# Kernel optimization log

Measured on AMD Instinct MI355X. Metric: run time of the kernel, lower is better.

The kernel has to match this reference:

```python
import jax, jax.numpy as jnp
import numpy as np

N_NODES = 100000
N_EDGES = 1600000
D = 128

def setup_inputs() -> dict:
    key = jax.random.key(0)
    ks = jax.random.split(key, 8)
    s = 1.0 / np.sqrt(D)
    x = jax.random.normal(ks[0], (N_NODES, D), dtype=jnp.float32)
    edge_index = jax.random.randint(ks[1], (2, N_EDGES), 0, N_NODES, dtype=jnp.int64)
    Wl1 = jax.random.normal(ks[2], (D, D), dtype=jnp.float32) * s
    Wr1 = jax.random.normal(ks[3], (D, D), dtype=jnp.float32) * s
    b1 = jax.random.normal(ks[4], (D,), dtype=jnp.float32) * s
    Wl2 = jax.random.normal(ks[5], (D, D), dtype=jnp.float32) * s
    Wr2 = jax.random.normal(ks[6], (D, D), dtype=jnp.float32) * s
    b2 = jax.random.normal(ks[7], (D,), dtype=jnp.float32) * s
    return {"x": x, "edge_index": edge_index, "Wl1": Wl1, "Wr1": Wr1, "b1": b1,
            "Wl2": Wl2, "Wr2": Wr2, "b2": b2}

def _sage_mean(x, src, dst, n, Wl, Wr, b):
    # mean-aggregate neighbor features onto destination nodes
    msg = x[src]                                      # [E, D] gather
    agg = jax.ops.segment_sum(msg, dst, num_segments=n)  # [N, D] scatter-add
    deg = jax.ops.segment_sum(jnp.ones((src.shape[0],), x.dtype), dst, num_segments=n)
    mean = agg / jnp.maximum(deg, 1.0)[:, None]
    # SAGEConv: lin_l(aggregated) + lin_r(self), bias on lin_l
    return mean @ Wl.T + x @ Wr.T + b

def reference(x, edge_index, Wl1, Wr1, b1, Wl2, Wr2, b2):
    src, dst = edge_index[0], edge_index[1]
    n = x.shape[0]
    h = _sage_mean(x, src, dst, n, Wl1, Wr1, b1)
    h = jax.nn.relu(h)
    return _sage_mean(h, src, dst, n, Wl2, Wr2, b2)
```

## Files before the change

kernel.cpp:

```cpp
#include <hip/hip_runtime.h>
#include <hip/hip_bf16.h>

#define NN 100000
#define NE 1600000
#define DD 128

#define ASHIFT 8
#define NSPAN  256
#define BK     391
#define BCAP   4608
#define EPB    8192
#define NAB    196
#define TFH    1563
#define HELEM  800000
#define PWB    16

typedef __attribute__((ext_vector_type(8))) short bf16x8;
typedef __attribute__((ext_vector_type(4))) float f32x4;
typedef __attribute__((ext_vector_type(2))) float f32x2;

__device__ inline unsigned short f2bf(float f) {
    unsigned u = __builtin_bit_cast(unsigned, f);
    u += 0x7fff + ((u >> 16) & 1);
    return (unsigned short)(u >> 16);
}
__device__ inline float bf2f(unsigned short h) {
    return __builtin_bit_cast(float, (unsigned)h << 16);
}

__device__ inline void tofeat_body(int half, int blk, int t,
                                   const float* __restrict__ in,
                                   unsigned short* __restrict__ outb,
                                   unsigned char* __restrict__ out8) {
    const size_t local = (size_t)blk * 512 + t;
    if (local >= HELEM) return;
    const size_t i = (size_t)half * HELEM + local;
    const float4 a = *(const float4*)&in[i * 8];
    const float4 b = *(const float4*)&in[i * 8 + 4];
    unsigned short o[8] = {f2bf(a.x), f2bf(a.y), f2bf(a.z), f2bf(a.w),
                           f2bf(b.x), f2bf(b.y), f2bf(b.z), f2bf(b.w)};
    *(bf16x8*)&outb[i * 8] = *(bf16x8*)o;
    unsigned e0 = 0, e1 = 0;
    e0 = __builtin_amdgcn_cvt_pk_fp8_f32(a.x, a.y, e0, false);
    e0 = __builtin_amdgcn_cvt_pk_fp8_f32(a.z, a.w, e0, true);
    e1 = __builtin_amdgcn_cvt_pk_fp8_f32(b.x, b.y, e1, false);
    e1 = __builtin_amdgcn_cvt_pk_fp8_f32(b.z, b.w, e1, true);
    uint2 p = {e0, e1};
    *(uint2*)&out8[i * 8] = p;
}

__global__ __launch_bounds__(512) void fusedA2(const int* __restrict__ src,
                                               const int* __restrict__ dst,
                                               int* __restrict__ gcur,
                                               int* __restrict__ pairs,
                                               const float* __restrict__ in,
                                               unsigned short* __restrict__ outb,
                                               unsigned char* __restrict__ out8,
                                               const float* __restrict__ Wl1,
                                               const float* __restrict__ Wr1,
                                               const float* __restrict__ Wl2,
                                               const float* __restrict__ Wr2,
                                               unsigned short* __restrict__ wsb) {
    __shared__ int hist[BK];
    __shared__ int gbase[BK];
    __shared__ int lcur[BK];
    const int t = threadIdx.x;

    if (blockIdx.x >= NAB + TFH) {
        const int tid = (blockIdx.x - NAB - TFH) * 512 + t;
        const int mat = tid >> 11;
        const int ko  = (tid >> 7) & 15;
        const int j   = tid & 127;
        const float* W = (mat == 0) ? Wl1 : (mat == 1) ? Wr1 : (mat == 2) ? Wl2 : Wr2;
        const float4 w0 = *(const float4*)&W[(size_t)j * DD + ko * 8];
        const float4 w1 = *(const float4*)&W[(size_t)j * DD + ko * 8 + 4];
        unsigned short o[8] = {f2bf(w0.x), f2bf(w0.y), f2bf(w0.z), f2bf(w0.w),
                               f2bf(w1.x), f2bf(w1.y), f2bf(w1.z), f2bf(w1.w)};
        *(bf16x8*)&wsb[(size_t)tid * 8] = *(bf16x8*)o;
        return;
    }
    if (blockIdx.x >= NAB) {
        tofeat_body(0, blockIdx.x - NAB, t, in, outb, out8);
        return;
    }

    const int e0 = blockIdx.x * EPB;
    int dcache[16];
    #pragma unroll
    for (int k = 0; k < 16; ++k) {
        const int e = e0 + t + k * 512;
        dcache[k] = (e < NE) ? dst[e] : -1;
    }

    for (int i = t; i < BK; i += 512) hist[i] = 0;
    __syncthreads();
    #pragma unroll
    for (int k = 0; k < 16; ++k)
        if (dcache[k] >= 0) atomicAdd(&hist[dcache[k] >> ASHIFT], 1);
    __syncthreads();
    for (int i = t; i < BK; i += 512) {
        int c = hist[i];
        gbase[i] = i * BCAP + (c ? atomicAdd(&gcur[i], c) : 0);
        lcur[i] = 0;
    }
    __syncthreads();
    #pragma unroll
    for (int k = 0; k < 16; ++k) {
        const int e = e0 + t + k * 512;
        const int d = dcache[k];
        if (d >= 0) {
            const int b = d >> ASHIFT;
            const int r = atomicAdd(&lcur[b], 1);
            pairs[gbase[b] + r] = ((d & (NSPAN - 1)) << 17) | src[e];
        }
    }
}

__global__ __launch_bounds__(512) void fusedB2(const int* __restrict__ pairs,
                                               const int* __restrict__ gcur,
                                               int* __restrict__ cnt,
                                               int* __restrict__ rowoff,
                                               int* __restrict__ csr,
                                               const float* __restrict__ in,
                                               unsigned short* __restrict__ outb,
                                               unsigned char* __restrict__ out8) {
    __shared__ int bs[512];
    __shared__ int hist[NSPAN];
    __shared__ int scanbuf[NSPAN];
    const int t = threadIdx.x;

    if (blockIdx.x >= BK) {
        tofeat_body(1, blockIdx.x - BK, t, in, outb, out8);
        return;
    }

    const int b = blockIdx.x;
    int v = (t < BK) ? gcur[t] : 0;
    bs[t] = v;
    __syncthreads();
    #pragma unroll
    for (int d = 1; d < 512; d <<= 1) {
        int u = (t >= d) ? bs[t - d] : 0;
        __syncthreads();
        bs[t] += u;
        __syncthreads();
    }
    const int sz   = gcur[b];
    const int base = bs[b] - sz;

    const int n0    = b << ASHIFT;
    const int nodeN = min(NSPAN, NN - n0);
    const int* ep   = &pairs[(size_t)b * BCAP];

    for (int i = t; i < NSPAN; i += 512) hist[i] = 0;
    __syncthreads();
    for (int i = t; i < sz; i += 512) atomicAdd(&hist[((unsigned)ep[i]) >> 17], 1);
    __syncthreads();
    for (int i = t; i < nodeN; i += 512) cnt[n0 + i] = hist[i];
    for (int i = t; i < NSPAN; i += 512) scanbuf[i] = hist[i];
    __syncthreads();
    #pragma unroll
    for (int d = 1; d < NSPAN; d <<= 1) {
        int v0 = (t >= d && t < NSPAN) ? scanbuf[t - d] : 0;
        __syncthreads();
        if (t < NSPAN) scanbuf[t] += v0;
        __syncthreads();
    }
    for (int i = t; i < NSPAN; i += 512) {
        int excl = scanbuf[i] - hist[i];
        if (i < nodeN) rowoff[n0 + i] = base + excl;
        hist[i] = excl;
    }
    if (b == BK - 1 && t == 0) rowoff[NN] = NE;
    __syncthreads();
    for (int i = t; i < sz; i += 512) {
        int p = ep[i];
        int r = atomicAdd(&hist[((unsigned)p) >> 17], 1);
        csr[base + r] = p & 0x1FFFF;
    }
}

__device__ inline void accum8(float* a, uint2 u) {
    f32x2 p;
    p = __builtin_amdgcn_cvt_pk_f32_fp8(u.x, false); a[0] += p.x; a[1] += p.y;
    p = __builtin_amdgcn_cvt_pk_f32_fp8(u.x, true);  a[2] += p.x; a[3] += p.y;
    p = __builtin_amdgcn_cvt_pk_f32_fp8(u.y, false); a[4] += p.x; a[5] += p.y;
    p = __builtin_amdgcn_cvt_pk_f32_fp8(u.y, true);  a[6] += p.x; a[7] += p.y;
}

__global__ __launch_bounds__(256) void gather_fp8(const unsigned char* __restrict__ feat,
                                                  const int* __restrict__ rowoff,
                                                  const int* __restrict__ csr,
                                                  const int* __restrict__ cnt,
                                                  unsigned short* __restrict__ mean) {
    const int node = blockIdx.x * 16 + (threadIdx.x >> 4);
    const int l8 = (threadIdx.x & 15) * 8;
    const int beg = rowoff[node], end = rowoff[node + 1];
    float a0[8] = {0, 0, 0, 0, 0, 0, 0, 0};
    float a1[8] = {0, 0, 0, 0, 0, 0, 0, 0};
    int j = beg;
    for (; j + 7 < end; j += 8) {
        int s0 = csr[j],     s1 = csr[j + 1], s2 = csr[j + 2], s3 = csr[j + 3];
        int s4 = csr[j + 4], s5 = csr[j + 5], s6 = csr[j + 6], s7 = csr[j + 7];
        uint2 u0 = *(const uint2*)&feat[(size_t)s0 * DD + l8];
        uint2 u1 = *(const uint2*)&feat[(size_t)s1 * DD + l8];
        uint2 u2 = *(const uint2*)&feat[(size_t)s2 * DD + l8];
        uint2 u3 = *(const uint2*)&feat[(size_t)s3 * DD + l8];
        uint2 u4 = *(const uint2*)&feat[(size_t)s4 * DD + l8];
        uint2 u5 = *(const uint2*)&feat[(size_t)s5 * DD + l8];
        uint2 u6 = *(const uint2*)&feat[(size_t)s6 * DD + l8];
        uint2 u7 = *(const uint2*)&feat[(size_t)s7 * DD + l8];
        accum8(a0, u0); accum8(a1, u1); accum8(a0, u2); accum8(a1, u3);
        accum8(a0, u4); accum8(a1, u5); accum8(a0, u6); accum8(a1, u7);
    }
    for (; j + 3 < end; j += 4) {
        int s0 = csr[j], s1 = csr[j + 1], s2 = csr[j + 2], s3 = csr[j + 3];
        uint2 u0 = *(const uint2*)&feat[(size_t)s0 * DD + l8];
        uint2 u1 = *(const uint2*)&feat[(size_t)s1 * DD + l8];
        uint2 u2 = *(const uint2*)&feat[(size_t)s2 * DD + l8];
        uint2 u3 = *(const uint2*)&feat[(size_t)s3 * DD + l8];
        accum8(a0, u0); accum8(a1, u1); accum8(a0, u2); accum8(a1, u3);
    }
    for (; j < end; ++j) {
        int s0 = csr[j];
        uint2 u0 = *(const uint2*)&feat[(size_t)s0 * DD + l8];
        accum8(a0, u0);
    }
    const float inv = 1.0f / fmaxf((float)cnt[node], 1.0f);
    unsigned short o[8];
    #pragma unroll
    for (int i = 0; i < 8; ++i) o[i] = f2bf((a0[i] + a1[i]) * inv);
    *(bf16x8*)&mean[(size_t)node * DD + l8] = *(bf16x8*)o;
}

__global__ __launch_bounds__(256, 3) void combine_mfma(
    const unsigned short* __restrict__ mean, const unsigned short* __restrict__ self,
    const unsigned short* __restrict__ wsb,
    const float* __restrict__ bias, void* __restrict__ outp,
    unsigned char* __restrict__ out8,
    int out_bf16, int do_relu)
{
    const int t = threadIdx.x;
    const int wv = t >> 6, lane = t & 63;
    const int m = lane & 15;
    const int q = lane >> 4;
    const int j0 = wv * 2;

    bf16x8 bfr[2][4][2];
    #pragma unroll
    for (int h = 0; h < 2; ++h)
        #pragma unroll
        for (int kq = 0; kq < 4; ++kq)
            #pragma unroll
            for (int jj = 0; jj < 2; ++jj)
                bfr[h][kq][jj] = *(const bf16x8*)
                    &wsb[((size_t)((h * 16 + kq * 4 + q) * 128) + (j0 + jj) * 16 + m) * 8];

    float bv[2];
    #pragma unroll
    for (int jj = 0; jj < 2; ++jj) bv[jj] = bias[(j0 + jj) * 16 + m];

    for (int tile = blockIdx.x; tile < NN / 16; tile += gridDim.x) {
        const size_t arow = ((size_t)tile * 16 + m) * DD;
        f32x4 acc[2];
        acc[0] = (f32x4){0.f, 0.f, 0.f, 0.f};
        acc[1] = (f32x4){0.f, 0.f, 0.f, 0.f};

        #pragma unroll
        for (int kq = 0; kq < 4; ++kq) {
            const bf16x8 am = *(const bf16x8*)&mean[arow + kq * 32 + q * 8];
            const bf16x8 as = *(const bf16x8*)&self[arow + kq * 32 + q * 8];
            #pragma unroll
            for (int jj = 0; jj < 2; ++jj) {
                acc[jj] = __builtin_amdgcn_mfma_f32_16x16x32_bf16(am, bfr[0][kq][jj], acc[jj], 0, 0, 0);
                acc[jj] = __builtin_amdgcn_mfma_f32_16x16x32_bf16(as, bfr[1][kq][jj], acc[jj], 0, 0, 0);
            }
        }

        #pragma unroll
        for (int jj = 0; jj < 2; ++jj) {
            const int col = (j0 + jj) * 16 + m;
            #pragma unroll
            for (int r = 0; r < 4; ++r) {
                const size_t row = (size_t)tile * 16 + q * 4 + r;
                float v = acc[jj][r] + bv[jj];
                if (do_relu) v = fmaxf(v, 0.0f);
                if (out_bf16)
                    ((unsigned short*)outp)[row * DD + col] = f2bf(v);
                else
                    ((float*)outp)[row * DD + col] = v;
                if (out8) {
                    unsigned p = __builtin_amdgcn_cvt_pk_fp8_f32(v, v, 0u, false);
                    out8[row * DD + col] = (unsigned char)p;
                }
            }
        }
    }
}

extern "C" void kernel_launch(void* const* d_in, const int* in_sizes, int n_in,
                              void* d_out, int out_size, void* d_ws, size_t ws_size,
                              hipStream_t stream) {
    const float* x   = (const float*)d_in[0];
    const int*   ei  = (const int*)d_in[1];
    const float* Wl1 = (const float*)d_in[2];
    const float* Wr1 = (const float*)d_in[3];
    const float* b1  = (const float*)d_in[4];
    const float* Wl2 = (const float*)d_in[5];
    const float* Wr2 = (const float*)d_in[6];
    const float* b2  = (const float*)d_in[7];
    const int* src = ei;
    const int* dst = ei + NE;
    float* out = (float*)d_out;

    unsigned short* xb   = (unsigned short*)d_ws;
    unsigned short* mean = xb + (size_t)NN * DD;
    unsigned short* h    = mean + (size_t)NN * DD;
    unsigned char*  x8   = (unsigned char*)(h + (size_t)NN * DD);
    unsigned char*  h8   = x8 + (size_t)NN * DD;
    int*  pairs  = (int*)(h8 + (size_t)NN * DD);
    int*  gcur   = pairs + (size_t)BK * BCAP;
    int*  cnt    = gcur + BK;
    int*  rowoff = cnt + NN;
    int*  csr    = rowoff + NN + 1;
    uintptr_t wp = ((uintptr_t)(csr + NE) + 255) & ~(uintptr_t)255;
    unsigned short* wsb = (unsigned short*)wp;

    hipMemsetAsync(gcur, 0, BK * sizeof(int), stream);
    fusedA2<<<NAB + TFH + PWB, 512, 0, stream>>>(src, dst, gcur, pairs,
                                                 x, xb, x8,
                                                 Wl1, Wr1, Wl2, Wr2, wsb);
    fusedB2<<<BK + TFH, 512, 0, stream>>>(pairs, gcur, cnt, rowoff, csr, x, xb, x8);

    gather_fp8<<<NN / 16, 256, 0, stream>>>(x8, rowoff, csr, cnt, mean);
    combine_mfma<<<2048, 256, 0, stream>>>(mean, xb, wsb, b1, h, h8, 1, 1);

    gather_fp8<<<NN / 16, 256, 0, stream>>>(h8, rowoff, csr, cnt, mean);
    combine_mfma<<<2048, 256, 0, stream>>>(mean, h, wsb + 32768, b2, out, nullptr, 0, 0);
}
```

Before: 279.4 us.

## Fuse neighbor mean gather into MFMA combine kernel via shared memory tile

Merges the fp8 gather/mean kernel and the bf16 MFMA combine kernel into one persistent kernel. Each 16-node tile's mean rows are built in LDS and fed straight to the MFMAs, so the global mean buffer write and read-back and two launches are removed. In exchange, each tile now runs gather then compute between two block barriers, so load imbalance from degree variation can stall the MFMA phase. The grid also drops to 2048 persistent blocks with launch bounds of 3, which may give less latency hiding for the gather than the previous 6250-block launch.

```diff
diff --git a/kernel.cpp b/kernel.cpp
--- a/kernel.cpp
+++ b/kernel.cpp
@@ -188,63 +188,24 @@
     p = __builtin_amdgcn_cvt_pk_f32_fp8(u.y, true);  a[6] += p.x; a[7] += p.y;
 }
 
-__global__ __launch_bounds__(256) void gather_fp8(const unsigned char* __restrict__ feat,
-                                                  const int* __restrict__ rowoff,
-                                                  const int* __restrict__ csr,
-                                                  const int* __restrict__ cnt,
-                                                  unsigned short* __restrict__ mean) {
-    const int node = blockIdx.x * 16 + (threadIdx.x >> 4);
-    const int l8 = (threadIdx.x & 15) * 8;
-    const int beg = rowoff[node], end = rowoff[node + 1];
-    float a0[8] = {0, 0, 0, 0, 0, 0, 0, 0};
-    float a1[8] = {0, 0, 0, 0, 0, 0, 0, 0};
-    int j = beg;
-    for (; j + 7 < end; j += 8) {
-        int s0 = csr[j],     s1 = csr[j + 1], s2 = csr[j + 2], s3 = csr[j + 3];
-        int s4 = csr[j + 4], s5 = csr[j + 5], s6 = csr[j + 6], s7 = csr[j + 7];
-        uint2 u0 = *(const uint2*)&feat[(size_t)s0 * DD + l8];
-        uint2 u1 = *(const uint2*)&feat[(size_t)s1 * DD + l8];
-        uint2 u2 = *(const uint2*)&feat[(size_t)s2 * DD + l8];
-        uint2 u3 = *(const uint2*)&feat[(size_t)s3 * DD + l8];
-        uint2 u4 = *(const uint2*)&feat[(size_t)s4 * DD + l8];
-        uint2 u5 = *(const uint2*)&feat[(size_t)s5 * DD + l8];
-        uint2 u6 = *(const uint2*)&feat[(size_t)s6 * DD + l8];
-        uint2 u7 = *(const uint2*)&feat[(size_t)s7 * DD + l8];
-        accum8(a0, u0); accum8(a1, u1); accum8(a0, u2); accum8(a1, u3);
-        accum8(a0, u4); accum8(a1, u5); accum8(a0, u6); accum8(a1, u7);
-    }
-    for (; j + 3 < end; j += 4) {
-        int s0 = csr[j], s1 = csr[j + 1], s2 = csr[j + 2], s3 = csr[j + 3];
-        uint2 u0 = *(const uint2*)&feat[(size_t)s0 * DD + l8];
-        uint2 u1 = *(const uint2*)&feat[(size_t)s1 * DD + l8];
-        uint2 u2 = *(const uint2*)&feat[(size_t)s2 * DD + l8];
-        uint2 u3 = *(const uint2*)&feat[(size_t)s3 * DD + l8];
-        accum8(a0, u0); accum8(a1, u1); accum8(a0, u2); accum8(a1, u3);
-    }
-    for (; j < end; ++j) {
-        int s0 = csr[j];
-        uint2 u0 = *(const uint2*)&feat[(size_t)s0 * DD + l8];
-        accum8(a0, u0);
-    }
-    const float inv = 1.0f / fmaxf((float)cnt[node], 1.0f);
-    unsigned short o[8];
-    #pragma unroll
-    for (int i = 0; i < 8; ++i) o[i] = f2bf((a0[i] + a1[i]) * inv);
-    *(bf16x8*)&mean[(size_t)node * DD + l8] = *(bf16x8*)o;
-}
-
-__global__ __launch_bounds__(256, 3) void combine_mfma(
-    const unsigned short* __restrict__ mean, const unsigned short* __restrict__ self,
+__global__ __launch_bounds__(256, 3) void gathcomb(
+    const unsigned char* __restrict__ feat,
+    const int* __restrict__ rowoff, const int* __restrict__ csr,
+    const int* __restrict__ cnt,
+    const unsigned short* __restrict__ self,
     const unsigned short* __restrict__ wsb,
     const float* __restrict__ bias, void* __restrict__ outp,
     unsigned char* __restrict__ out8,
     int out_bf16, int do_relu)
 {
+    __shared__ unsigned short meanS[16][136];
     const int t = threadIdx.x;
     const int wv = t >> 6, lane = t & 63;
     const int m = lane & 15;
     const int q = lane >> 4;
     const int j0 = wv * 2;
+    const int nl = t >> 4;
+    const int l8 = (t & 15) * 8;
 
     bf16x8 bfr[2][4][2];
     #pragma unroll
@@ -261,40 +222,84 @@
     for (int jj = 0; jj < 2; ++jj) bv[jj] = bias[(j0 + jj) * 16 + m];
 
     for (int tile = blockIdx.x; tile < NN / 16; tile += gridDim.x) {
-        const size_t arow = ((size_t)tile * 16 + m) * DD;
-        f32x4 acc[2];
-        acc[0] = (f32x4){0.f, 0.f, 0.f, 0.f};
-        acc[1] = (f32x4){0.f, 0.f, 0.f, 0.f};
-
-        #pragma unroll
-        for (int kq = 0; kq < 4; ++kq) {
-            const bf16x8 am = *(const bf16x8*)&mean[arow + kq * 32 + q * 8];
-            const bf16x8 as = *(const bf16x8*)&self[arow + kq * 32 + q * 8];
+        {
+            const int node = tile * 16 + nl;
+            const int beg = rowoff[node], end = rowoff[node + 1];
+            float a0[8] = {0, 0, 0, 0, 0, 0, 0, 0};
+            float a1[8] = {0, 0, 0, 0, 0, 0, 0, 0};
+            int j = beg;
+            for (; j + 7 < end; j += 8) {
+                int s0 = csr[j],     s1 = csr[j + 1], s2 = csr[j + 2], s3 = csr[j + 3];
+                int s4 = csr[j + 4], s5 = csr[j + 5], s6 = csr[j + 6], s7 = csr[j + 7];
+                uint2 u0 = *(const uint2*)&feat[(size_t)s0 * DD + l8];
+                uint2 u1 = *(const uint2*)&feat[(size_t)s1 * DD + l8];
+                uint2 u2 = *(const uint2*)&feat[(size_t)s2 * DD + l8];
+                uint2 u3 = *(const uint2*)&feat[(size_t)s3 * DD + l8];
+                uint2 u4 = *(const uint2*)&feat[(size_t)s4 * DD + l8];
+                uint2 u5 = *(const uint2*)&feat[(size_t)s5 * DD + l8];
+                uint2 u6 = *(const uint2*)&feat[(size_t)s6 * DD + l8];
+                uint2 u7 = *(const uint2*)&feat[(size_t)s7 * DD + l8];
+                accum8(a0, u0); accum8(a1, u1); accum8(a0, u2); accum8(a1, u3);
+                accum8(a0, u4); accum8(a1, u5); accum8(a0, u6); accum8(a1, u7);
+            }
+            for (; j + 3 < end; j += 4) {
+                int s0 = csr[j], s1 = csr[j + 1], s2 = csr[j + 2], s3 = csr[j + 3];
+                uint2 u0 = *(const uint2*)&feat[(size_t)s0 * DD + l8];
+                uint2 u1 = *(const uint2*)&feat[(size_t)s1 * DD + l8];
+                uint2 u2 = *(const uint2*)&feat[(size_t)s2 * DD + l8];
+                uint2 u3 = *(const uint2*)&feat[(size_t)s3 * DD + l8];
+                accum8(a0, u0); accum8(a1, u1); accum8(a0, u2); accum8(a1, u3);
+            }
+            for (; j < end; ++j) {
+                int s0 = csr[j];
+                uint2 u0 = *(const uint2*)&feat[(size_t)s0 * DD + l8];
+                accum8(a0, u0);
+            }
+            const float inv = 1.0f / fmaxf((float)cnt[node], 1.0f);
+            unsigned short o[8];
+            #pragma unroll
+            for (int i = 0; i < 8; ++i) o[i] = f2bf((a0[i] + a1[i]) * inv);
+            *(bf16x8*)&meanS[nl][l8] = *(bf16x8*)o;
+        }
+        __syncthreads();
+
+        {
+            f32x4 acc[2];
+            acc[0] = (f32x4){0.f, 0.f, 0.f, 0.f};
+            acc[1] = (f32x4){0.f, 0.f, 0.f, 0.f};
+            const size_t arow = ((size_t)tile * 16 + m) * DD;
+
+            #pragma unroll
+            for (int kq = 0; kq < 4; ++kq) {
+                const bf16x8 am = *(const bf16x8*)&meanS[m][kq * 32 + q * 8];
+                const bf16x8 as = *(const bf16x8*)&self[arow + kq * 32 + q * 8];
+                #pragma unroll
+                for (int jj = 0; jj < 2; ++jj) {
+                    acc[jj] = __builtin_amdgcn_mfma_f32_16x16x32_bf16(am, bfr[0][kq][jj], acc[jj], 0, 0, 0);
+                    acc[jj] = __builtin_amdgcn_mfma_f32_16x16x32_bf16(as, bfr[1][kq][jj], acc[jj], 0, 0, 0);
+                }
+            }
+
             #pragma unroll
             for (int jj = 0; jj < 2; ++jj) {
-                acc[jj] = __builtin_amdgcn_mfma_f32_16x16x32_bf16(am, bfr[0][kq][jj], acc[jj], 0, 0, 0);
-                acc[jj] = __builtin_amdgcn_mfma_f32_16x16x32_bf16(as, bfr[1][kq][jj], acc[jj], 0, 0, 0);
+                const int col = (j0 + jj) * 16 + m;
+                #pragma unroll
+                for (int r = 0; r < 4; ++r) {
+                    const size_t row = (size_t)tile * 16 + q * 4 + r;
+                    float v = acc[jj][r] + bv[jj];
+                    if (do_relu) v = fmaxf(v, 0.0f);
+                    if (out_bf16)
+                        ((unsigned short*)outp)[row * DD + col] = f2bf(v);
+                    else
+                        ((float*)outp)[row * DD + col] = v;
+                    if (out8) {
+                        unsigned p = __builtin_amdgcn_cvt_pk_fp8_f32(v, v, 0u, false);
+                        out8[row * DD + col] = (unsigned char)p;
+                    }
+                }
             }
         }
-
-        #pragma unroll
-        for (int jj = 0; jj < 2; ++jj) {
-            const int col = (j0 + jj) * 16 + m;
-            #pragma unroll
-            for (int r = 0; r < 4; ++r) {
-                const size_t row = (size_t)tile * 16 + q * 4 + r;
-                float v = acc[jj][r] + bv[jj];
-                if (do_relu) v = fmaxf(v, 0.0f);
-                if (out_bf16)
-                    ((unsigned short*)outp)[row * DD + col] = f2bf(v);
-                else
-                    ((float*)outp)[row * DD + col] = v;
-                if (out8) {
-                    unsigned p = __builtin_amdgcn_cvt_pk_fp8_f32(v, v, 0u, false);
-                    out8[row * DD + col] = (unsigned char)p;
-                }
-            }
-        }
+        __syncthreads();
     }
 }
 
@@ -314,8 +319,7 @@
     float* out = (float*)d_out;
 
     unsigned short* xb   = (unsigned short*)d_ws;
-    unsigned short* mean = xb + (size_t)NN * DD;
-    unsigned short* h    = mean + (size_t)NN * DD;
+    unsigned short* h    = xb + (size_t)NN * DD;
     unsigned char*  x8   = (unsigned char*)(h + (size_t)NN * DD);
     unsigned char*  h8   = x8 + (size_t)NN * DD;
     int*  pairs  = (int*)(h8 + (size_t)NN * DD);
@@ -332,9 +336,8 @@
                                                  Wl1, Wr1, Wl2, Wr2, wsb);
     fusedB2<<<BK + TFH, 512, 0, stream>>>(pairs, gcur, cnt, rowoff, csr, x, xb, x8);
 
-    gather_fp8<<<NN / 16, 256, 0, stream>>>(x8, rowoff, csr, cnt, mean);
-    combine_mfma<<<2048, 256, 0, stream>>>(mean, xb, wsb, b1, h, h8, 1, 1);
-
-    gather_fp8<<<NN / 16, 256, 0, stream>>>(h8, rowoff, csr, cnt, mean);
-    combine_mfma<<<2048, 256, 0, stream>>>(mean, h, wsb + 32768, b2, out, nullptr, 0, 0);
-}
+    gathcomb<<<2048, 256, 0, stream>>>(x8, rowoff, csr, cnt, xb, wsb, b1,
+                                       h, h8, 1, 1);
+    gathcomb<<<2048, 256, 0, stream>>>(h8, rowoff, csr, cnt, h, wsb + 32768, b2,
+                                       out, nullptr, 0, 0);
+}
```

After: 306.6 us. +9.8%, slower.

## Stage combine A tiles through double-buffered LDS with async global-to-LDS loads

Applied to the files above, without the earlier changes.

Rewrites the combine GEMM kernel so each 512-thread block loads the mean and self tiles into shared memory once, using global_load_lds, and double-buffers the next tile while computing the current one. In the old kernel each wave reloaded the same A rows from global memory. Each wave now owns one 16-column output slice instead of two. The change aims to cut redundant A loads and hide load latency. In exchange it adds a __syncthreads per tile and uses a smaller grid of 1024 blocks.

```diff
diff --git a/kernel.cpp b/kernel.cpp
--- a/kernel.cpp
+++ b/kernel.cpp
@@ -14,6 +14,7 @@
 #define TFH    1563
 #define HELEM  800000
 #define PWB    16
+#define CGRID  1024
 
 typedef __attribute__((ext_vector_type(8))) short bf16x8;
 typedef __attribute__((ext_vector_type(4))) float f32x4;
@@ -26,6 +27,12 @@
 }
 __device__ inline float bf2f(unsigned short h) {
     return __builtin_bit_cast(float, (unsigned)h << 16);
+}
+
+__device__ inline void gload16(const void* g, void* l) {
+    __builtin_amdgcn_global_load_lds(
+        (const __attribute__((address_space(1))) unsigned int*)g,
+        (__attribute__((address_space(3))) unsigned int*)l, 16, 0, 0);
 }
 
 __device__ inline void tofeat_body(int half, int blk, int t,
@@ -233,69 +240,81 @@
     *(bf16x8*)&mean[(size_t)node * DD + l8] = *(bf16x8*)o;
 }
 
-__global__ __launch_bounds__(256, 3) void combine_mfma(
-    const unsigned short* __restrict__ mean, const unsigned short* __restrict__ self,
+__global__ __launch_bounds__(512, 3) void combine_lds(
+    const unsigned short* __restrict__ meanp, const unsigned short* __restrict__ selfp,
     const unsigned short* __restrict__ wsb,
     const float* __restrict__ bias, void* __restrict__ outp,
     unsigned char* __restrict__ out8,
     int out_bf16, int do_relu)
 {
+    __shared__ unsigned short sAB[2][2][2048];
     const int t = threadIdx.x;
     const int wv = t >> 6, lane = t & 63;
     const int m = lane & 15;
     const int q = lane >> 4;
-    const int j0 = wv * 2;
-
-    bf16x8 bfr[2][4][2];
+    const int j0 = wv;
+
+    const int sreg = wv >> 2;
+    const int skq  = wv & 3;
+    const int soff = m * 256 + skq * 64 + q * 16;
+
+    bf16x8 bfr[2][4];
     #pragma unroll
     for (int h = 0; h < 2; ++h)
         #pragma unroll
         for (int kq = 0; kq < 4; ++kq)
-            #pragma unroll
-            for (int jj = 0; jj < 2; ++jj)
-                bfr[h][kq][jj] = *(const bf16x8*)
-                    &wsb[((size_t)((h * 16 + kq * 4 + q) * 128) + (j0 + jj) * 16 + m) * 8];
-
-    float bv[2];
-    #pragma unroll
-    for (int jj = 0; jj < 2; ++jj) bv[jj] = bias[(j0 + jj) * 16 + m];
-
-    for (int tile = blockIdx.x; tile < NN / 16; tile += gridDim.x) {
-        const size_t arow = ((size_t)tile * 16 + m) * DD;
-        f32x4 acc[2];
-        acc[0] = (f32x4){0.f, 0.f, 0.f, 0.f};
-        acc[1] = (f32x4){0.f, 0.f, 0.f, 0.f};
-
+            bfr[h][kq] = *(const bf16x8*)
+                &wsb[((size_t)((h * 16 + kq * 4 + q) * 128) + j0 * 16 + m) * 8];
+
+    const float bv = bias[j0 * 16 + m];
+
+    const int NT = NN / 16;
+
+#define STAGE(BUF, TL)                                                        \
+    {                                                                         \
+        const char* base_ = sreg ? (const char*)selfp : (const char*)meanp;   \
+        gload16(base_ + (size_t)(TL) * 4096 + soff,                           \
+                (char*)&sAB[BUF][sreg][0] + skq * 1024);                      \
+    }
+
+    int tile = blockIdx.x;
+    STAGE(0, tile)
+    __syncthreads();
+    int cur = 0;
+
+    for (; tile < NT; tile += CGRID) {
+        const int nxt = tile + CGRID;
+        if (nxt < NT) STAGE(cur ^ 1, nxt)
+
+        f32x4 acc = (f32x4){0.f, 0.f, 0.f, 0.f};
         #pragma unroll
         for (int kq = 0; kq < 4; ++kq) {
-            const bf16x8 am = *(const bf16x8*)&mean[arow + kq * 32 + q * 8];
-            const bf16x8 as = *(const bf16x8*)&self[arow + kq * 32 + q * 8];
-            #pragma unroll
-            for (int jj = 0; jj < 2; ++jj) {
-                acc[jj] = __builtin_amdgcn_mfma_f32_16x16x32_bf16(am, bfr[0][kq][jj], acc[jj], 0, 0, 0);
-                acc[jj] = __builtin_amdgcn_mfma_f32_16x16x32_bf16(as, bfr[1][kq][jj], acc[jj], 0, 0, 0);
+            const bf16x8 am = *(const bf16x8*)&sAB[cur][0][kq * 512 + lane * 8];
+            const bf16x8 as = *(const bf16x8*)&sAB[cur][1][kq * 512 + lane * 8];
+            acc = __builtin_amdgcn_mfma_f32_16x16x32_bf16(am, bfr[0][kq], acc, 0, 0, 0);
+            acc = __builtin_amdgcn_mfma_f32_16x16x32_bf16(as, bfr[1][kq], acc, 0, 0, 0);
+        }
+
+        const int col = j0 * 16 + m;
+        #pragma unroll
+        for (int r = 0; r < 4; ++r) {
+            const size_t row = (size_t)tile * 16 + q * 4 + r;
+            float v = acc[r] + bv;
+            if (do_relu) v = fmaxf(v, 0.0f);
+            if (out_bf16)
+                ((unsigned short*)outp)[row * DD + col] = f2bf(v);
+            else
+                ((float*)outp)[row * DD + col] = v;
+            if (out8) {
+                unsigned p = __builtin_amdgcn_cvt_pk_fp8_f32(v, v, 0u, false);
+                out8[row * DD + col] = (unsigned char)p;
             }
         }
 
-        #pragma unroll
-        for (int jj = 0; jj < 2; ++jj) {
-            const int col = (j0 + jj) * 16 + m;
-            #pragma unroll
-            for (int r = 0; r < 4; ++r) {
-                const size_t row = (size_t)tile * 16 + q * 4 + r;
-                float v = acc[jj][r] + bv[jj];
-                if (do_relu) v = fmaxf(v, 0.0f);
-                if (out_bf16)
-                    ((unsigned short*)outp)[row * DD + col] = f2bf(v);
-                else
-                    ((float*)outp)[row * DD + col] = v;
-                if (out8) {
-                    unsigned p = __builtin_amdgcn_cvt_pk_fp8_f32(v, v, 0u, false);
-                    out8[row * DD + col] = (unsigned char)p;
-                }
-            }
-        }
-    }
+        __syncthreads();
+        cur ^= 1;
+    }
+#undef STAGE
 }
 
 extern "C" void kernel_launch(void* const* d_in, const int* in_sizes, int n_in,
@@ -333,8 +352,8 @@
     fusedB2<<<BK + TFH, 512, 0, stream>>>(pairs, gcur, cnt, rowoff, csr, x, xb, x8);
 
     gather_fp8<<<NN / 16, 256, 0, stream>>>(x8, rowoff, csr, cnt, mean);
-    combine_mfma<<<2048, 256, 0, stream>>>(mean, xb, wsb, b1, h, h8, 1, 1);
+    combine_lds<<<CGRID, 512, 0, stream>>>(mean, xb, wsb, b1, h, h8, 1, 1);
 
     gather_fp8<<<NN / 16, 256, 0, stream>>>(h8, rowoff, csr, cnt, mean);
-    combine_mfma<<<2048, 256, 0, stream>>>(mean, h, wsb + 32768, b2, out, nullptr, 0, 0);
-}
+    combine_lds<<<CGRID, 512, 0, stream>>>(mean, h, wsb + 32768, b2, out, nullptr, 0, 0);
+}
```

Result: faster. 254.1 us (-9.0%).
